# Kernel optimization log

Measured on AMD Instinct MI355X. Metric: run time of the kernel, lower is better.

The kernel has to match this reference:

```python
import jax, jax.numpy as jnp
import numpy as np
import math

V, D, NHEAD, NHID, NLAYERS = 50258, 1024, 8, 2048, 2
NUIDS, B, S, TOPK = 2000, 4, 256, 20


def layer_norm(x, g, b):
    m = x.mean(-1, keepdims=True)
    v = ((x - m) ** 2).mean(-1, keepdims=True)
    return (x - m) / jnp.sqrt(v + 1e-5) * g + b


def mha(x, Wqkv, bqkv, Wo, bo):
    Bx, Sx, Dx = x.shape
    hd = Dx // NHEAD
    qkv = x @ Wqkv.T + bqkv                       # [B,S,3D]
    q, k, v = jnp.split(qkv, 3, axis=-1)
    q = q.reshape(Bx, Sx, NHEAD, hd)
    k = k.reshape(Bx, Sx, NHEAD, hd)
    v = v.reshape(Bx, Sx, NHEAD, hd)
    att = jnp.einsum('bqhd,bkhd->bhqk', q, k) / math.sqrt(hd)
    att = jax.nn.softmax(att, axis=-1)
    o = jnp.einsum('bhqk,bkhd->bqhd', att, v).reshape(Bx, Sx, Dx)
    return o @ Wo.T + bo


def enc_layer(x, Wqkv, bqkv, Wo, bo, W1, b1, W2, b2, g1, be1, g2, be2):
    # torch TransformerEncoderLayer, post-LN, relu, dropout=0 (eval)
    x = layer_norm(x + mha(x, Wqkv, bqkv, Wo, bo), g1, be1)
    ff = jax.nn.relu(x @ W1.T + b1) @ W2.T + b2
    return layer_norm(x + ff, g2, be2)


def setup_inputs() -> dict:
    key = jax.random.key(0)
    ks = jax.random.split(key, 32)
    s = 0.02
    inp = {
        'inputs': jax.random.randint(ks[0], (B, S), 0, V),
        'uids': jnp.arange(NUIDS),
        'noise': jax.random.normal(ks[1], (NUIDS,), dtype=jnp.float32),
        'responses_hidden': jax.random.normal(ks[2], (B, S, D), dtype=jnp.float32),
        'topk': TOPK,
        'emb': jax.random.normal(ks[3], (V, D), dtype=jnp.float32) * s,
        # routing encoder (1 layer)
        'r_Wqkv': jax.random.normal(ks[4], (3 * D, D)) * s,
        'r_bqkv': jnp.zeros((3 * D,)),
        'r_Wo': jax.random.normal(ks[5], (D, D)) * s,
        'r_bo': jnp.zeros((D,)),
        'r_W1': jax.random.normal(ks[6], (NHID, D)) * s,
        'r_b1': jnp.zeros((NHID,)),
        'r_W2': jax.random.normal(ks[7], (D, NHID)) * s,
        'r_b2': jnp.zeros((D,)),
        'r_ln1g': jnp.ones((D,)), 'r_ln1b': jnp.zeros((D,)),
        'r_ln2g': jnp.ones((D,)), 'r_ln2b': jnp.zeros((D,)),
        # main encoder (NLAYERS, stacked)
        'e_Wqkv': jax.random.normal(ks[8], (NLAYERS, 3 * D, D)) * s,
        'e_bqkv': jnp.zeros((NLAYERS, 3 * D)),
        'e_Wo': jax.random.normal(ks[9], (NLAYERS, D, D)) * s,
        'e_bo': jnp.zeros((NLAYERS, D)),
        'e_W1': jax.random.normal(ks[10], (NLAYERS, NHID, D)) * s,
        'e_b1': jnp.zeros((NLAYERS, NHID)),
        'e_W2': jax.random.normal(ks[11], (NLAYERS, D, NHID)) * s,
        'e_b2': jnp.zeros((NLAYERS, D)),
        'e_ln1g': jnp.ones((NLAYERS, D)), 'e_ln1b': jnp.zeros((NLAYERS, D)),
        'e_ln2g': jnp.ones((NLAYERS, D)), 'e_ln2b': jnp.zeros((NLAYERS, D)),
        'dec_W': jax.random.normal(ks[12], (V, D)) * s,
        # 2000 tiny gates fused into one [NUIDS, D] matmul
        'gate_W': jax.random.normal(ks[13], (NUIDS, D)) * s,
        'gate_b': jnp.zeros((NUIDS,)),
    }
    return inp


def reference(inputs, uids, noise, responses_hidden, topk, emb,
              r_Wqkv, r_bqkv, r_Wo, r_bo, r_W1, r_b1, r_W2, r_b2,
              r_ln1g, r_ln1b, r_ln2g, r_ln2b,
              e_Wqkv, e_bqkv, e_Wo, e_bo, e_W1, e_b1, e_W2, e_b2,
              e_ln1g, e_ln1b, e_ln2g, e_ln2b,
              dec_W, gate_W, gate_b):
    # --- routing path ---
    h = emb[inputs]                                            # [B,S,D]
    rc = enc_layer(h, r_Wqkv, r_bqkv, r_Wo, r_bo, r_W1, r_b1,
                   r_W2, r_b2, r_ln1g, r_ln1b, r_ln2g, r_ln2b)
    rc = rc * math.sqrt(D)
    # fused per-UID gates: 2000 Linear(D,1) -> one [B,NUIDS] matmul
    rw = rc[:, -1, :] @ gate_W.T + gate_b                      # [B,NUIDS]
    bw = rw.mean(axis=0)                                       # [NUIDS]
    noisy = noise * jnp.std(bw)
    full = jnp.zeros((NUIDS,), dtype=bw.dtype).at[uids].set(bw + noisy)
    topk_w, topk_uids = jax.lax.top_k(full, topk)
    # --- target loss on joined responses ---
    x = responses_hidden
    for l in range(NLAYERS):
        x = enc_layer(x, e_Wqkv[l], e_bqkv[l], e_Wo[l], e_bo[l],
                      e_W1[l], e_b1[l], e_W2[l], e_b2[l],
                      e_ln1g[l], e_ln1b[l], e_ln2g[l], e_ln2b[l])
    logits = x @ dec_W.T                                       # [B,S,V]
    shift_logits = logits[:, :-1, :].reshape(-1, V)
    shift_labels = inputs[:, 1:].reshape(-1)
    logp = jax.nn.log_softmax(shift_logits, axis=-1)
    loss = -jnp.take_along_axis(logp, shift_labels[:, None], axis=1).mean()
    return loss, topk_w, topk_uids
```

## Files before the change

### kernel.cpp

```cpp
#include <hip/hip_runtime.h>

typedef unsigned short ushort_t;
typedef __bf16 bf16x8_t __attribute__((ext_vector_type(8)));
typedef float f32x4_t __attribute__((ext_vector_type(4)));

#define AS1(p) ((const __attribute__((address_space(1))) void*)(p))
#define AS3(p) ((__attribute__((address_space(3))) void*)(p))
#define DEVINL __device__ __forceinline__

DEVINL ushort_t f2bf(float f) {
    unsigned int u = __builtin_bit_cast(unsigned int, f);
    u += 0x7fffu + ((u >> 16) & 1u);
    return (ushort_t)(u >> 16);
}
DEVINL float bf2f(ushort_t h) {
    unsigned int u = ((unsigned int)h) << 16;
    return __builtin_bit_cast(float, u);
}

DEVINL float warp_sum(float v) {
#pragma unroll
    for (int o = 32; o > 0; o >>= 1) v += __shfl_xor(v, o);
    return v;
}
DEVINL float warp_max(float v) {
#pragma unroll
    for (int o = 32; o > 0; o >>= 1) v = fmaxf(v, __shfl_xor(v, o));
    return v;
}
DEVINL float block_sum(float v, float* sb) {
    v = warp_sum(v);
    int w = threadIdx.x >> 6;
    if ((threadIdx.x & 63) == 0) sb[w] = v;
    __syncthreads();
    v = sb[0] + sb[1] + sb[2] + sb[3];
    __syncthreads();
    return v;
}
DEVINL float block_max(float v, float* sb) {
    v = warp_max(v);
    int w = threadIdx.x >> 6;
    if ((threadIdx.x & 63) == 0) sb[w] = v;
    __syncthreads();
    v = fmaxf(fmaxf(sb[0], sb[1]), fmaxf(sb[2], sb[3]));
    __syncthreads();
    return v;
}

template <int EPI>
__global__ __launch_bounds__(256) void gemm_bt(
    const ushort_t* __restrict__ A, long lda, long sA1, long sA2,
    const ushort_t* __restrict__ B, long ldb, long sB1, long sB2,
    void* __restrict__ Cp, long ldc, long sC1, long sC2,
    const float* __restrict__ bias, int accum, int K, int batch2)
{
    __shared__ __align__(16) __bf16 As[128 * 32];
    __shared__ __align__(16) __bf16 Bs[128 * 32];

    const int tid = threadIdx.x;
    const int lane = tid & 63;
    const int wave = tid >> 6;
    const int wm = wave >> 1, wn = wave & 1;
    const int quad = lane >> 4, l16 = lane & 15;
    const long m0 = (long)blockIdx.y * 128;
    const long n0 = (long)blockIdx.x * 128;
    const int z = blockIdx.z;
    const int z1 = z / batch2, z2 = z % batch2;
    A += (long)z1 * sA1 + (long)z2 * sA2;
    B += (long)z1 * sB1 + (long)z2 * sB2;

    f32x4_t acc[4][4];
#pragma unroll
    for (int i = 0; i < 4; i++)
#pragma unroll
        for (int j = 0; j < 4; j++) {
            f32x4_t zv = {0.f, 0.f, 0.f, 0.f};
            acc[i][j] = zv;
        }

    const int ea = tid * 8;
    const int nkt = K >> 5;
    for (int kt = 0; kt < nkt; ++kt) {
        const int k0 = kt << 5;
#pragma unroll
        for (int inst = 0; inst < 2; ++inst) {
            int e = ea + inst * 2048;
            int row = e >> 5, kk = e & 31;
            __builtin_amdgcn_global_load_lds(AS1(A + (m0 + row) * lda + k0 + kk), AS3(As + e), 16, 0, 0);
            __builtin_amdgcn_global_load_lds(AS1(B + (n0 + row) * ldb + k0 + kk), AS3(Bs + e), 16, 0, 0);
        }
        __syncthreads();
        bf16x8_t af[4], bfr[4];
#pragma unroll
        for (int i = 0; i < 4; i++)
            af[i] = *(const bf16x8_t*)(As + (wm * 64 + i * 16 + l16) * 32 + quad * 8);
#pragma unroll
        for (int j = 0; j < 4; j++)
            bfr[j] = *(const bf16x8_t*)(Bs + (wn * 64 + j * 16 + l16) * 32 + quad * 8);
#pragma unroll
        for (int i = 0; i < 4; i++)
#pragma unroll
            for (int j = 0; j < 4; j++)
                acc[i][j] = __builtin_amdgcn_mfma_f32_16x16x32_bf16(af[i], bfr[j], acc[i][j], 0, 0, 0);
        __syncthreads();
    }

    if constexpr (EPI == 0) {
        float* C = (float*)Cp + (long)z1 * sC1 + (long)z2 * sC2;
#pragma unroll
        for (int i = 0; i < 4; i++)
#pragma unroll
            for (int reg = 0; reg < 4; reg++) {
                long row = m0 + wm * 64 + i * 16 + quad * 4 + reg;
#pragma unroll
                for (int j = 0; j < 4; j++) {
                    long col = n0 + wn * 64 + j * 16 + l16;
                    float v = acc[i][j][reg];
                    if (bias) v += bias[col];
                    long idx = row * ldc + col;
                    if (accum) v += C[idx];
                    C[idx] = v;
                }
            }
    } else {
        ushort_t* C = (ushort_t*)Cp + (long)z1 * sC1 + (long)z2 * sC2;
#pragma unroll
        for (int i = 0; i < 4; i++)
#pragma unroll
            for (int reg = 0; reg < 4; reg++) {
                long row = m0 + wm * 64 + i * 16 + quad * 4 + reg;
#pragma unroll
                for (int j = 0; j < 4; j++) {
                    long col = n0 + wn * 64 + j * 16 + l16;
                    float v = acc[i][j][reg];
                    if (bias) v += bias[col];
                    if constexpr (EPI == 2) v = fmaxf(v, 0.f);
                    C[row * ldc + col] = f2bf(v);
                }
            }
    }
}

__global__ __launch_bounds__(256) void gemm_split(
    const ushort_t* __restrict__ Ah, const ushort_t* __restrict__ Al, long lda,
    const ushort_t* __restrict__ Bh, const ushort_t* __restrict__ Bl, long ldb,
    float* __restrict__ C, long ldc, const float* __restrict__ bias, int K)
{
    __shared__ __align__(16) __bf16 Ahs[4096], Als[4096], Bhs[4096], Bls[4096];
    const int tid = threadIdx.x;
    const int lane = tid & 63;
    const int wave = tid >> 6;
    const int wm = wave >> 1, wn = wave & 1;
    const int quad = lane >> 4, l16 = lane & 15;
    const long m0 = (long)blockIdx.y * 128;
    const long n0 = (long)blockIdx.x * 128;

    f32x4_t acc[4][4];
#pragma unroll
    for (int i = 0; i < 4; i++)
#pragma unroll
        for (int j = 0; j < 4; j++) {
            f32x4_t zv = {0.f, 0.f, 0.f, 0.f};
            acc[i][j] = zv;
        }

    const int ea = tid * 8;
    const int nkt = K >> 5;
    for (int kt = 0; kt < nkt; ++kt) {
        const int k0 = kt << 5;
#pragma unroll
        for (int inst = 0; inst < 2; ++inst) {
            int e = ea + inst * 2048;
            int row = e >> 5, kk = e & 31;
            long ao = (m0 + row) * lda + k0 + kk;
            long bo = (n0 + row) * ldb + k0 + kk;
            __builtin_amdgcn_global_load_lds(AS1(Ah + ao), AS3(Ahs + e), 16, 0, 0);
            __builtin_amdgcn_global_load_lds(AS1(Al + ao), AS3(Als + e), 16, 0, 0);
            __builtin_amdgcn_global_load_lds(AS1(Bh + bo), AS3(Bhs + e), 16, 0, 0);
            __builtin_amdgcn_global_load_lds(AS1(Bl + bo), AS3(Bls + e), 16, 0, 0);
        }
        __syncthreads();
        bf16x8_t ah[4], al[4], bh[4], bl[4];
#pragma unroll
        for (int i = 0; i < 4; i++) {
            int off = (wm * 64 + i * 16 + l16) * 32 + quad * 8;
            ah[i] = *(const bf16x8_t*)(Ahs + off);
            al[i] = *(const bf16x8_t*)(Als + off);
        }
#pragma unroll
        for (int j = 0; j < 4; j++) {
            int off = (wn * 64 + j * 16 + l16) * 32 + quad * 8;
            bh[j] = *(const bf16x8_t*)(Bhs + off);
            bl[j] = *(const bf16x8_t*)(Bls + off);
        }
#pragma unroll
        for (int i = 0; i < 4; i++)
#pragma unroll
            for (int j = 0; j < 4; j++) {
                acc[i][j] = __builtin_amdgcn_mfma_f32_16x16x32_bf16(al[i], bh[j], acc[i][j], 0, 0, 0);
                acc[i][j] = __builtin_amdgcn_mfma_f32_16x16x32_bf16(ah[i], bl[j], acc[i][j], 0, 0, 0);
                acc[i][j] = __builtin_amdgcn_mfma_f32_16x16x32_bf16(ah[i], bh[j], acc[i][j], 0, 0, 0);
            }
        __syncthreads();
    }

#pragma unroll
    for (int i = 0; i < 4; i++)
#pragma unroll
        for (int reg = 0; reg < 4; reg++) {
            long row = m0 + wm * 64 + i * 16 + quad * 4 + reg;
#pragma unroll
            for (int j = 0; j < 4; j++) {
                long col = n0 + wn * 64 + j * 16 + l16;
                C[row * ldc + col] = acc[i][j][reg] + bias[col];
            }
        }
}

__global__ __launch_bounds__(256) void gemm_ce(
    const ushort_t* __restrict__ A, long lda,
    const ushort_t* __restrict__ B, long ldb,
    int K, int n_real, const int* __restrict__ inputs,
    float* __restrict__ part_m, float* __restrict__ part_s,
    float* __restrict__ label_logit)
{
    __shared__ __align__(16) __bf16 As[128 * 32];
    __shared__ __align__(16) __bf16 Bs[128 * 32];

    const int tid = threadIdx.x;
    const int lane = tid & 63;
    const int wave = tid >> 6;
    const int wm = wave >> 1, wn = wave & 1;
    const int quad = lane >> 4, l16 = lane & 15;
    const long m0 = (long)blockIdx.x * 128;
    const long n0 = (long)blockIdx.y * 128;

    f32x4_t acc[4][4];
#pragma unroll
    for (int i = 0; i < 4; i++)
#pragma unroll
        for (int j = 0; j < 4; j++) {
            f32x4_t zv = {0.f, 0.f, 0.f, 0.f};
            acc[i][j] = zv;
        }

    const int ea = tid * 8;
    const int nkt = K >> 5;
    for (int kt = 0; kt < nkt; ++kt) {
        const int k0 = kt << 5;
#pragma unroll
        for (int inst = 0; inst < 2; ++inst) {
            int e = ea + inst * 2048;
            int row = e >> 5, kk = e & 31;
            __builtin_amdgcn_global_load_lds(AS1(A + (m0 + row) * lda + k0 + kk), AS3(As + e), 16, 0, 0);
            __builtin_amdgcn_global_load_lds(AS1(B + (n0 + row) * ldb + k0 + kk), AS3(Bs + e), 16, 0, 0);
        }
        __syncthreads();
        bf16x8_t af[4], bfr[4];
#pragma unroll
        for (int i = 0; i < 4; i++)
            af[i] = *(const bf16x8_t*)(As + (wm * 64 + i * 16 + l16) * 32 + quad * 8);
#pragma unroll
        for (int j = 0; j < 4; j++)
            bfr[j] = *(const bf16x8_t*)(Bs + (wn * 64 + j * 16 + l16) * 32 + quad * 8);
#pragma unroll
        for (int i = 0; i < 4; i++)
#pragma unroll
            for (int j = 0; j < 4; j++)
                acc[i][j] = __builtin_amdgcn_mfma_f32_16x16x32_bf16(af[i], bfr[j], acc[i][j], 0, 0, 0);
        __syncthreads();
    }

#pragma unroll
    for (int i = 0; i < 4; i++) {
#pragma unroll
        for (int reg = 0; reg < 4; reg++) {
            long row = m0 + wm * 64 + i * 16 + quad * 4 + reg;
            int lab = ((row & 255) == 255) ? -1 : inputs[row + 1];
            float mx = -INFINITY;
#pragma unroll
            for (int j = 0; j < 4; j++) {
                long col = n0 + wn * 64 + j * 16 + l16;
                float v = acc[i][j][reg];
                if (col < n_real) mx = fmaxf(mx, v);
            }
#pragma unroll
            for (int o = 8; o > 0; o >>= 1) mx = fmaxf(mx, __shfl_xor(mx, o));
            float sm = 0.f;
#pragma unroll
            for (int j = 0; j < 4; j++) {
                long col = n0 + wn * 64 + j * 16 + l16;
                float v = acc[i][j][reg];
                if (col < n_real) sm += __expf(v - mx);
                if (col == lab) label_logit[row] = v;
            }
#pragma unroll
            for (int o = 8; o > 0; o >>= 1) sm += __shfl_xor(sm, o);
            if (l16 == 0) {
                long pidx = row * 786 + (long)blockIdx.y * 2 + wn;
                part_m[pidx] = mx;
                part_s[pidx] = sm;
            }
        }
    }
}


__global__ __launch_bounds__(256) void k_convert_seg(
    const float* __restrict__ s0, ushort_t* __restrict__ d0, long n0,
    const float* __restrict__ s1, ushort_t* __restrict__ d1, long n1,
    const float* __restrict__ s2, ushort_t* __restrict__ d2, long n2,
    const float* __restrict__ s3, ushort_t* __restrict__ d3, long n3,
    const float* __restrict__ s4, ushort_t* __restrict__ d4, long n4)
{
    long i = ((long)blockIdx.x * 256 + threadIdx.x) * 4;
    const float* src; ushort_t* dst;
    if (i < n0) { src = s0; dst = d0; }
    else if ((i -= n0) < n1) { src = s1; dst = d1; }
    else if ((i -= n1) < n2) { src = s2; dst = d2; }
    else if ((i -= n2) < n3) { src = s3; dst = d3; }
    else if ((i -= n3) < n4) { src = s4; dst = d4; }
    else return;
    float4 v = *(const float4*)(src + i);
    dst[i + 0] = f2bf(v.x); dst[i + 1] = f2bf(v.y);
    dst[i + 2] = f2bf(v.z); dst[i + 3] = f2bf(v.w);
}

__global__ __launch_bounds__(256) void k_convert_pad(const float* __restrict__ src,
                                                     ushort_t* __restrict__ dst,
                                                     long n_src, long n_dst) {
    long i = ((long)blockIdx.x * 256 + threadIdx.x) * 4;
    if (i >= n_dst) return;
    if (i < n_src) {
        float4 v = *(const float4*)(src + i);
        dst[i + 0] = f2bf(v.x); dst[i + 1] = f2bf(v.y);
        dst[i + 2] = f2bf(v.z); dst[i + 3] = f2bf(v.w);
    } else {
        dst[i + 0] = 0; dst[i + 1] = 0; dst[i + 2] = 0; dst[i + 3] = 0;
    }
}

__global__ __launch_bounds__(256) void k_convert2(const float* __restrict__ src,
                                                  ushort_t* __restrict__ hi,
                                                  ushort_t* __restrict__ lo, long n) {
    long i = ((long)blockIdx.x * 256 + threadIdx.x) * 4;
    if (i >= n) return;
    float4 v = *(const float4*)(src + i);
    float vv[4] = {v.x, v.y, v.z, v.w};
#pragma unroll
    for (int j = 0; j < 4; j++) {
        ushort_t h = f2bf(vv[j]);
        hi[i + j] = h;
        lo[i + j] = f2bf(vv[j] - bf2f(h));
    }
}

__global__ __launch_bounds__(256) void k_gather2(const int* __restrict__ inputs,
                                                 const float* __restrict__ emb,
                                                 ushort_t* __restrict__ hi,
                                                 ushort_t* __restrict__ lo,
                                                 float* __restrict__ loss_out) {
    int t = blockIdx.x, tid = threadIdx.x;
    if (t == 0 && tid == 0) loss_out[0] = 0.f;
    long row = inputs[t];
    float4 v = *(const float4*)(emb + row * 1024 + tid * 4);
    long base = (long)t * 1024 + tid * 4;
    float vv[4] = {v.x, v.y, v.z, v.w};
#pragma unroll
    for (int j = 0; j < 4; j++) {
        ushort_t h = f2bf(vv[j]);
        hi[base + j] = h;
        lo[base + j] = f2bf(vv[j] - bf2f(h));
    }
}

__global__ __launch_bounds__(256) void k_rq(
    const int* __restrict__ inputs, const float* __restrict__ emb,
    const float* __restrict__ Wq, const float* __restrict__ bq,
    float* __restrict__ qf)
{
    __shared__ __align__(16) float xs[4096];
    int tid = threadIdx.x;
#pragma unroll
    for (int b2 = 0; b2 < 4; b2++) {
        long tok = inputs[b2 * 256 + 255];
        *(float4*)(xs + b2 * 1024 + tid * 4) = *(const float4*)(emb + tok * 1024 + tid * 4);
    }
    __syncthreads();
    int wave = tid >> 6, lane = tid & 63;
    int d = blockIdx.x * 4 + wave;
    const float4* wr = (const float4*)(Wq + (long)d * 1024) + lane * 4;
    const float4* x0 = (const float4*)xs + lane * 4;
    const float4* x1 = (const float4*)(xs + 1024) + lane * 4;
    const float4* x2 = (const float4*)(xs + 2048) + lane * 4;
    const float4* x3 = (const float4*)(xs + 3072) + lane * 4;
    float a0 = 0, a1 = 0, a2 = 0, a3 = 0;
#pragma unroll
    for (int k = 0; k < 4; k++) {
        float4 w = wr[k];
        float4 v0 = x0[k], v1 = x1[k], v2 = x2[k], v3 = x3[k];
        a0 += w.x * v0.x + w.y * v0.y + w.z * v0.z + w.w * v0.w;
        a1 += w.x * v1.x + w.y * v1.y + w.z * v1.z + w.w * v1.w;
        a2 += w.x * v2.x + w.y * v2.y + w.z * v2.z + w.w * v2.w;
        a3 += w.x * v3.x + w.y * v3.y + w.z * v3.z + w.w * v3.w;
    }
    a0 = warp_sum(a0); a1 = warp_sum(a1); a2 = warp_sum(a2); a3 = warp_sum(a3);
    if (lane < 4) {
        float a = (lane == 0) ? a0 : (lane == 1) ? a1 : (lane == 2) ? a2 : a3;
        qf[lane * 1024 + d] = a + bq[d];
    }
}

__global__ __launch_bounds__(256) void k_rattn(const float* __restrict__ qf,
                                               const float* __restrict__ kv,
                                               float* __restrict__ o_rt) {
    int zz = blockIdx.x, b = zz >> 3, h = zz & 7, tid = threadIdx.x;
    __shared__ __align__(16) float q[128];
    __shared__ float p[256];
    __shared__ float sb[8];
    if (tid < 128) q[tid] = qf[b * 1024 + h * 128 + tid];
    __syncthreads();
    const float4* q4 = (const float4*)q;
    const float4* kr = (const float4*)(kv + ((long)(b * 256 + tid)) * 2048 + h * 128);
    float a = 0.f;
#pragma unroll 8
    for (int k = 0; k < 32; k++) {
        float4 wv = kr[k], xv = q4[k];
        a += wv.x * xv.x + wv.y * xv.y + wv.z * xv.z + wv.w * xv.w;
    }
    a *= 0.08838834764831845f;
    float m = block_max(a, sb);
    float e = __expf(a - m);
    float ssum = block_sum(e, sb);
    p[tid] = e / ssum;
    __syncthreads();
    if (tid < 128) {
        float acc = 0.f;
        const float* vb = kv + (long)b * 256 * 2048 + 1024 + h * 128 + tid;
        for (int s = 0; s < 256; s++) acc += p[s] * vb[(long)s * 2048];
        o_rt[b * 1024 + h * 128 + tid] = acc;
    }
}

__global__ __launch_bounds__(256) void k_rwo(
    const float* __restrict__ o_rt, const int* __restrict__ inputs,
    const float* __restrict__ emb, const float* __restrict__ Wo,
    const float* __restrict__ bo, float* __restrict__ rbuf)
{
    __shared__ __align__(16) float xs[4096];
    int tid = threadIdx.x;
#pragma unroll
    for (int i = 0; i < 16; i++) xs[i * 256 + tid] = o_rt[i * 256 + tid];
    __syncthreads();
    int wave = tid >> 6, lane = tid & 63;
    int d = blockIdx.x * 4 + wave;
    const float4* wr = (const float4*)(Wo + (long)d * 1024) + lane * 4;
    const float4* x0 = (const float4*)xs + lane * 4;
    const float4* x1 = (const float4*)(xs + 1024) + lane * 4;
    const float4* x2 = (const float4*)(xs + 2048) + lane * 4;
    const float4* x3 = (const float4*)(xs + 3072) + lane * 4;
    float a0 = 0, a1 = 0, a2 = 0, a3 = 0;
#pragma unroll
    for (int k = 0; k < 4; k++) {
        float4 w = wr[k];
        float4 v0 = x0[k], v1 = x1[k], v2 = x2[k], v3 = x3[k];
        a0 += w.x * v0.x + w.y * v0.y + w.z * v0.z + w.w * v0.w;
        a1 += w.x * v1.x + w.y * v1.y + w.z * v1.z + w.w * v1.w;
        a2 += w.x * v2.x + w.y * v2.y + w.z * v2.z + w.w * v2.w;
        a3 += w.x * v3.x + w.y * v3.y + w.z * v3.z + w.w * v3.w;
    }
    a0 = warp_sum(a0); a1 = warp_sum(a1); a2 = warp_sum(a2); a3 = warp_sum(a3);
    if (lane < 4) {
        float a = (lane == 0) ? a0 : (lane == 1) ? a1 : (lane == 2) ? a2 : a3;
        long tok = inputs[lane * 256 + 255];
        rbuf[lane * 1024 + d] = emb[tok * 1024 + d] + bo[d] + a;
    }
}

__global__ __launch_bounds__(256) void k_rln(const float* __restrict__ r,
                                             const float* __restrict__ g,
                                             const float* __restrict__ be,
                                             float* __restrict__ outp, float scale) {
    int row = blockIdx.x, tid = threadIdx.x;
    __shared__ float sb[8];
    const float* rr = r + (long)row * 1024;
    float v[4], s = 0.f, sq = 0.f;
#pragma unroll
    for (int i = 0; i < 4; i++) {
        v[i] = rr[i * 256 + tid];
        s += v[i]; sq += v[i] * v[i];
    }
    s = block_sum(s, sb); sq = block_sum(sq, sb + 4);
    float mean = s * (1.f / 1024.f);
    float rstd = rsqrtf(sq * (1.f / 1024.f) - mean * mean + 1e-5f);
#pragma unroll
    for (int i = 0; i < 4; i++) {
        int d = i * 256 + tid;
        outp[(long)row * 1024 + d] = ((v[i] - mean) * rstd * g[d] + be[d]) * scale;
    }
}

__global__ __launch_bounds__(256) void k_rff1(
    const float* __restrict__ x1f, const float* __restrict__ W1,
    const float* __restrict__ b1, float* __restrict__ f1f)
{
    __shared__ __align__(16) float xs[4096];
    int tid = threadIdx.x;
#pragma unroll
    for (int i = 0; i < 16; i++) xs[i * 256 + tid] = x1f[i * 256 + tid];
    __syncthreads();
    int wave = tid >> 6, lane = tid & 63;
    int j = blockIdx.x * 4 + wave;
    const float4* wr = (const float4*)(W1 + (long)j * 1024) + lane * 4;
    const float4* x0 = (const float4*)xs + lane * 4;
    const float4* x1 = (const float4*)(xs + 1024) + lane * 4;
    const float4* x2 = (const float4*)(xs + 2048) + lane * 4;
    const float4* x3 = (const float4*)(xs + 3072) + lane * 4;
    float a0 = 0, a1 = 0, a2 = 0, a3 = 0;
#pragma unroll
    for (int k = 0; k < 4; k++) {
        float4 w = wr[k];
        float4 v0 = x0[k], v1 = x1[k], v2 = x2[k], v3 = x3[k];
        a0 += w.x * v0.x + w.y * v0.y + w.z * v0.z + w.w * v0.w;
        a1 += w.x * v1.x + w.y * v1.y + w.z * v1.z + w.w * v1.w;
        a2 += w.x * v2.x + w.y * v2.y + w.z * v2.z + w.w * v2.w;
        a3 += w.x * v3.x + w.y * v3.y + w.z * v3.z + w.w * v3.w;
    }
    a0 = warp_sum(a0); a1 = warp_sum(a1); a2 = warp_sum(a2); a3 = warp_sum(a3);
    if (lane < 4) {
        float a = (lane == 0) ? a0 : (lane == 1) ? a1 : (lane == 2) ? a2 : a3;
        f1f[lane * 2048 + j] = fmaxf(b1[j] + a, 0.f);
    }
}

__global__ __launch_bounds__(256) void k_rff2(
    const float* __restrict__ f1f, const float* __restrict__ x1f,
    const float* __restrict__ W2, const float* __restrict__ b2,
    float* __restrict__ r2f)
{
    __shared__ __align__(16) float xs[8192];
    int tid = threadIdx.x;
#pragma unroll
    for (int i = 0; i < 32; i++) xs[i * 256 + tid] = f1f[i * 256 + tid];
    __syncthreads();
    int wave = tid >> 6, lane = tid & 63;
    int d = blockIdx.x * 4 + wave;
    const float4* wr = (const float4*)(W2 + (long)d * 2048) + lane * 8;
    const float4* x0 = (const float4*)xs + lane * 8;
    const float4* x1 = (const float4*)(xs + 2048) + lane * 8;
    const float4* x2 = (const float4*)(xs + 4096) + lane * 8;
    const float4* x3 = (const float4*)(xs + 6144) + lane * 8;
    float a0 = 0, a1 = 0, a2 = 0, a3 = 0;
#pragma unroll
    for (int k = 0; k < 8; k++) {
        float4 w = wr[k];
        float4 v0 = x0[k], v1 = x1[k], v2 = x2[k], v3 = x3[k];
        a0 += w.x * v0.x + w.y * v0.y + w.z * v0.z + w.w * v0.w;
        a1 += w.x * v1.x + w.y * v1.y + w.z * v1.z + w.w * v1.w;
        a2 += w.x * v2.x + w.y * v2.y + w.z * v2.z + w.w * v2.w;
        a3 += w.x * v3.x + w.y * v3.y + w.z * v3.z + w.w * v3.w;
    }
    a0 = warp_sum(a0); a1 = warp_sum(a1); a2 = warp_sum(a2); a3 = warp_sum(a3);
    if (lane < 4) {
        float a = (lane == 0) ? a0 : (lane == 1) ? a1 : (lane == 2) ? a2 : a3;
        r2f[lane * 1024 + d] = x1f[lane * 1024 + d] + b2[d] + a;
    }
}

__global__ __launch_bounds__(256) void k_gate(const float* __restrict__ rc,
                                              const float* __restrict__ gw,
                                              const float* __restrict__ gb,
                                              float* __restrict__ bw) {
    __shared__ __align__(16) float xs[4096];
    int tid = threadIdx.x;
#pragma unroll
    for (int i = 0; i < 16; i++) xs[i * 256 + tid] = rc[i * 256 + tid];
    __syncthreads();
    int wave = tid >> 6, lane = tid & 63;
    int u = blockIdx.x * 4 + wave;
    const float4* wr = (const float4*)(gw + (long)u * 1024) + lane * 4;
    const float4* x0 = (const float4*)xs + lane * 4;
    const float4* x1 = (const float4*)(xs + 1024) + lane * 4;
    const float4* x2 = (const float4*)(xs + 2048) + lane * 4;
    const float4* x3 = (const float4*)(xs + 3072) + lane * 4;
    float a0 = 0, a1 = 0, a2 = 0, a3 = 0;
#pragma unroll
    for (int k = 0; k < 4; k++) {
        float4 w = wr[k];
        float4 v0 = x0[k], v1 = x1[k], v2 = x2[k], v3 = x3[k];
        a0 += w.x * v0.x + w.y * v0.y + w.z * v0.z + w.w * v0.w;
        a1 += w.x * v1.x + w.y * v1.y + w.z * v1.z + w.w * v1.w;
        a2 += w.x * v2.x + w.y * v2.y + w.z * v2.z + w.w * v2.w;
        a3 += w.x * v3.x + w.y * v3.y + w.z * v3.z + w.w * v3.w;
    }
    a0 = warp_sum(a0); a1 = warp_sum(a1); a2 = warp_sum(a2); a3 = warp_sum(a3);
    if (lane == 0)
        bw[u] = 0.25f * (a0 + a1 + a2 + a3) + gb[u];
}

__global__ __launch_bounds__(256) void k_topk(const float* __restrict__ bw,
                                              const int* __restrict__ uids,
                                              const float* __restrict__ noise,
                                              float* __restrict__ out) {
    int tid = threadIdx.x;
    __shared__ float full[2000];
    __shared__ float sb[8];
    __shared__ float rv[256];
    __shared__ int ri[256];
    float s = 0.f, sq = 0.f;
    for (int u = tid; u < 2000; u += 256) {
        float v = bw[u];
        s += v; sq += v * v;
    }
    s = block_sum(s, sb); sq = block_sum(sq, sb + 4);
    float mean = s * (1.f / 2000.f);
    float sd = sqrtf(fmaxf(sq * (1.f / 2000.f) - mean * mean, 0.f));
    for (int i = tid; i < 2000; i += 256) full[i] = 0.f;
    __syncthreads();
    for (int i = tid; i < 2000; i += 256) {
        int u = uids[i];
        if (u >= 0 && u < 2000) full[u] = bw[i] + noise[i] * sd;
    }
    __syncthreads();
    for (int it = 0; it < 20; ++it) {
        float bv = -INFINITY;
        int bi = 0x7fffffff;
        for (int i = tid; i < 2000; i += 256) {
            float v = full[i];
            if (v > bv || (v == bv && i < bi)) { bv = v; bi = i; }
        }
        rv[tid] = bv; ri[tid] = bi;
        __syncthreads();
        for (int stride = 128; stride > 0; stride >>= 1) {
            if (tid < stride) {
                float v2 = rv[tid + stride]; int i2 = ri[tid + stride];
                if (v2 > rv[tid] || (v2 == rv[tid] && i2 < ri[tid])) { rv[tid] = v2; ri[tid] = i2; }
            }
            __syncthreads();
        }
        if (tid == 0) {
            out[1 + it] = rv[0];
            out[21 + it] = (float)ri[0];
            full[ri[0]] = -INFINITY;
        }
        __syncthreads();
    }
}

__global__ __launch_bounds__(256) void k_vt(const ushort_t* __restrict__ qkv,
                                            ushort_t* __restrict__ vt) {
    int zz = blockIdx.y, b = zz >> 3, h = zz & 7;
    int s0 = blockIdx.x * 64, tid = threadIdx.x;
    __shared__ ushort_t t[64][130];
#pragma unroll
    for (int r = 0; r < 32; r++) {
        int idx = r * 256 + tid;
        int sl = idx >> 7, d = idx & 127;
        t[sl][d] = qkv[((long)(b * 256 + s0 + sl)) * 3072 + 2048 + h * 128 + d];
    }
    __syncthreads();
#pragma unroll
    for (int r = 0; r < 32; r++) {
        int idx = r * 256 + tid;
        int d = idx >> 6, sl = idx & 63;
        vt[((long)(zz * 128 + d)) * 256 + s0 + sl] = t[sl][d];
    }
}

__global__ void k_softmax(const float* __restrict__ S, ushort_t* __restrict__ P) {
    long row = blockIdx.x;
    int lane = threadIdx.x;
    const float* sr = S + row * 256;
    float v[4];
    float m = -INFINITY;
#pragma unroll
    for (int i = 0; i < 4; i++) {
        v[i] = sr[i * 64 + lane] * 0.08838834764831845f;
        m = fmaxf(m, v[i]);
    }
    m = warp_max(m);
    float s = 0.f;
#pragma unroll
    for (int i = 0; i < 4; i++) { v[i] = __expf(v[i] - m); s += v[i]; }
    s = warp_sum(s);
    float inv = 1.f / s;
#pragma unroll
    for (int i = 0; i < 4; i++) P[row * 256 + i * 64 + lane] = f2bf(v[i] * inv);
}

__global__ __launch_bounds__(256) void k_addln(const float* __restrict__ x,
                                               const float* __restrict__ y,
                                               const float* __restrict__ g,
                                               const float* __restrict__ b,
                                               float* __restrict__ xf,
                                               ushort_t* __restrict__ xb) {
    int row = blockIdx.x, tid = threadIdx.x;
    const float* xr = x + (long)row * 1024;
    const float* yr = y + (long)row * 1024;
    __shared__ float sb[8];
    float r[4], s = 0.f, sq = 0.f;
#pragma unroll
    for (int i = 0; i < 4; i++) {
        int d = i * 256 + tid;
        r[i] = xr[d] + yr[d];
        s += r[i]; sq += r[i] * r[i];
    }
    s = block_sum(s, sb); sq = block_sum(sq, sb + 4);
    float mean = s * (1.f / 1024.f);
    float rstd = rsqrtf(sq * (1.f / 1024.f) - mean * mean + 1e-5f);
#pragma unroll
    for (int i = 0; i < 4; i++) {
        int d = i * 256 + tid;
        float o = (r[i] - mean) * rstd * g[d] + b[d];
        xf[(long)row * 1024 + d] = o;
        xb[(long)row * 1024 + d] = f2bf(o);
    }
}

__global__ __launch_bounds__(256) void k_ce(const float* __restrict__ pm,
                                            const float* __restrict__ ps,
                                            const float* __restrict__ ll,
                                            const int* __restrict__ inputs,
                                            float* __restrict__ out) {
    const int NB = 786;
    long row = blockIdx.x;
    int tid = threadIdx.x;
    __shared__ float sb[8];
    float m = -INFINITY;
    for (int i = tid; i < NB; i += 256) m = fmaxf(m, pm[row * NB + i]);
    m = block_max(m, sb);
    float s = 0.f;
    for (int i = tid; i < NB; i += 256) s += ps[row * NB + i] * __expf(pm[row * NB + i] - m);
    s = block_sum(s, sb);
    if (tid == 0) {
        int lab = ((row & 255) == 255) ? -1 : inputs[row + 1];
        if (lab >= 0) atomicAdd(out, (m + logf(s) - ll[row]) * (1.0f / 1020.0f));
    }
}


extern "C" void kernel_launch(void* const* d_in, const int* in_sizes, int n_in,
                              void* d_out, int out_size, void* d_ws, size_t ws_size,
                              hipStream_t stream) {
    const int* inputs  = (const int*)d_in[0];
    const int* uids    = (const int*)d_in[1];
    const float* noise = (const float*)d_in[2];
    const float* resp  = (const float*)d_in[3];
    const float* emb   = (const float*)d_in[5];
    const float* r_Wqkv = (const float*)d_in[6];
    const float* r_bqkv = (const float*)d_in[7];
    const float* r_Wo = (const float*)d_in[8];
    const float* r_bo = (const float*)d_in[9];
    const float* r_W1 = (const float*)d_in[10];
    const float* r_b1 = (const float*)d_in[11];
    const float* r_W2 = (const float*)d_in[12];
    const float* r_b2 = (const float*)d_in[13];
    const float* r_ln1g = (const float*)d_in[14];
    const float* r_ln1b = (const float*)d_in[15];
    const float* r_ln2g = (const float*)d_in[16];
    const float* r_ln2b = (const float*)d_in[17];
    const float* e_Wqkv = (const float*)d_in[18];
    const float* e_bqkv = (const float*)d_in[19];
    const float* e_Wo = (const float*)d_in[20];
    const float* e_bo = (const float*)d_in[21];
    const float* e_W1 = (const float*)d_in[22];
    const float* e_b1 = (const float*)d_in[23];
    const float* e_W2 = (const float*)d_in[24];
    const float* e_b2 = (const float*)d_in[25];
    const float* e_ln1g = (const float*)d_in[26];
    const float* e_ln1b = (const float*)d_in[27];
    const float* e_ln2g = (const float*)d_in[28];
    const float* e_ln2b = (const float*)d_in[29];
    const float* dec_W = (const float*)d_in[30];
    const float* gate_W = (const float*)d_in[31];
    const float* gate_b = (const float*)d_in[32];
    float* out = (float*)d_out;
    (void)in_sizes; (void)n_in; (void)out_size; (void)ws_size;

    char* wp = (char*)d_ws;
    auto alloc = [&](size_t bytes) {
        char* p = wp;
        wp += (bytes + 255) & ~(size_t)255;
        return p;
    };
    ushort_t* wkv_hi = (ushort_t*)alloc(2097152ull * 2);
    ushort_t* wkv_lo = (ushort_t*)alloc(2097152ull * 2);
    ushort_t* wq_e = (ushort_t*)alloc(6291456ull * 2);
    ushort_t* wo_e = (ushort_t*)alloc(2097152ull * 2);
    ushort_t* w1_e = (ushort_t*)alloc(4194304ull * 2);
    ushort_t* w2_e = (ushort_t*)alloc(4194304ull * 2);
    ushort_t* decb = (ushort_t*)alloc(51511296ull * 2);
    ushort_t* h_hi = (ushort_t*)alloc(1048576ull * 2);
    ushort_t* h_lo = (ushort_t*)alloc(1048576ull * 2);
    float* qf = (float*)alloc(4096ull * 4);
    float* rkv = (float*)alloc(2097152ull * 4);
    float* o_rt = (float*)alloc(4096ull * 4);
    float* rbuf = (float*)alloc(4096ull * 4);
    float* x1f = (float*)alloc(4096ull * 4);
    float* f1f = (float*)alloc(8192ull * 4);
    float* r2f = (float*)alloc(4096ull * 4);
    float* rc = (float*)alloc(4096ull * 4);
    float* bw = (float*)alloc(2000ull * 4);
    ushort_t* xb = (ushort_t*)alloc(1048576ull * 2);
    float* xf = (float*)alloc(1048576ull * 4);
    ushort_t* qkvb = (ushort_t*)alloc(3145728ull * 2);
    ushort_t* vt = (ushort_t*)alloc(1048576ull * 2);
    float* Sb = (float*)alloc(2097152ull * 4);
    ushort_t* Pb = (ushort_t*)alloc(2097152ull * 2);
    ushort_t* ob = (ushort_t*)alloc(1048576ull * 2);
    float* tmpf = (float*)alloc(1048576ull * 4);
    ushort_t* ff1b = (ushort_t*)alloc(2097152ull * 2);
    float* pm = (float*)alloc(1024ull * 786 * 4);
    float* ps = (float*)alloc(1024ull * 786 * 4);
    float* ll = (float*)alloc(1024ull * 4);

    auto gemm = [&](int epi, const ushort_t* A_, long lda_, long sA1_, long sA2_,
                    const ushort_t* B_, long ldb_, long sB1_, long sB2_,
                    void* C_, long ldc_, long sC1_, long sC2_,
                    const float* bias_, int accum_, int M_, int N_, int K_,
                    int batch_, int batch2_) {
        dim3 g((unsigned)(N_ / 128), (unsigned)(M_ / 128), (unsigned)batch_);
        switch (epi) {
        case 0: gemm_bt<0><<<g, 256, 0, stream>>>(A_, lda_, sA1_, sA2_, B_, ldb_, sB1_, sB2_, C_, ldc_, sC1_, sC2_, bias_, accum_, K_, batch2_); break;
        case 1: gemm_bt<1><<<g, 256, 0, stream>>>(A_, lda_, sA1_, sA2_, B_, ldb_, sB1_, sB2_, C_, ldc_, sC1_, sC2_, bias_, accum_, K_, batch2_); break;
        case 2: gemm_bt<2><<<g, 256, 0, stream>>>(A_, lda_, sA1_, sA2_, B_, ldb_, sB1_, sB2_, C_, ldc_, sC1_, sC2_, bias_, accum_, K_, batch2_); break;
        }
    };

    k_convert_seg<<<17408, 256, 0, stream>>>(
        e_Wqkv, wq_e, 6291456L, e_Wo, wo_e, 2097152L, e_W1, w1_e, 4194304L,
        e_W2, w2_e, 4194304L, resp, xb, 1048576L);
    k_convert_pad<<<50304, 256, 0, stream>>>(dec_W, decb, 51464192L, 51511296L);
    k_convert2<<<2048, 256, 0, stream>>>(r_Wqkv + 1048576, wkv_hi, wkv_lo, 2097152L);
    k_gather2<<<1024, 256, 0, stream>>>(inputs, emb, h_hi, h_lo, out);

    k_rq<<<256, 256, 0, stream>>>(inputs, emb, r_Wqkv, r_bqkv, qf);
    {
        dim3 g(16, 8);
        gemm_split<<<g, 256, 0, stream>>>(h_hi, h_lo, 1024, wkv_hi, wkv_lo, 1024,
                                          rkv, 2048, r_bqkv + 1024, 1024);
    }
    k_rattn<<<32, 256, 0, stream>>>(qf, rkv, o_rt);
    k_rwo<<<256, 256, 0, stream>>>(o_rt, inputs, emb, r_Wo, r_bo, rbuf);
    k_rln<<<4, 256, 0, stream>>>(rbuf, r_ln1g, r_ln1b, x1f, 1.0f);
    k_rff1<<<512, 256, 0, stream>>>(x1f, r_W1, r_b1, f1f);
    k_rff2<<<256, 256, 0, stream>>>(f1f, x1f, r_W2, r_b2, r2f);
    k_rln<<<4, 256, 0, stream>>>(r2f, r_ln2g, r_ln2b, rc, 32.0f);
    k_gate<<<500, 256, 0, stream>>>(rc, gate_W, gate_b, bw);
    k_topk<<<1, 256, 0, stream>>>(bw, uids, noise, out);

    for (int l = 0; l < 2; ++l) {
        gemm(1, xb, 1024, 0, 0, wq_e + (size_t)l * 3145728, 1024, 0, 0, qkvb, 3072, 0, 0,
             e_bqkv + l * 3072, 0, 1024, 3072, 1024, 1, 1);
        k_vt<<<dim3(4, 32), 256, 0, stream>>>(qkvb, vt);
        gemm(0, qkvb, 3072, 786432, 128, qkvb + 1024, 3072, 786432, 128, Sb, 256, 524288, 65536,
             nullptr, 0, 256, 256, 128, 32, 8);
        k_softmax<<<8192, 64, 0, stream>>>(Sb, Pb);
        gemm(1, Pb, 256, 524288, 65536, vt, 256, 262144, 32768, ob, 1024, 262144, 128,
             nullptr, 0, 256, 128, 256, 32, 8);
        gemm(0, ob, 1024, 0, 0, wo_e + (size_t)l * 1048576, 1024, 0, 0, tmpf, 1024, 0, 0,
             e_bo + l * 1024, 0, 1024, 1024, 1024, 1, 1);
        k_addln<<<1024, 256, 0, stream>>>((l == 0) ? resp : (const float*)xf, tmpf,
                                          e_ln1g + l * 1024, e_ln1b + l * 1024, xf, xb);
        gemm(2, xb, 1024, 0, 0, w1_e + (size_t)l * 2097152, 1024, 0, 0, ff1b, 2048, 0, 0,
             e_b1 + l * 2048, 0, 1024, 2048, 1024, 1, 1);
        gemm(0, ff1b, 2048, 0, 0, w2_e + (size_t)l * 2097152, 2048, 0, 0, tmpf, 1024, 0, 0,
             e_b2 + l * 1024, 0, 1024, 1024, 2048, 1, 1);
        k_addln<<<1024, 256, 0, stream>>>(xf, tmpf, e_ln2g + l * 1024, e_ln2b + l * 1024, xf, xb);
    }

    {
        dim3 g(8, 393);
        gemm_ce<<<g, 256, 0, stream>>>(xb, 1024, decb, 1024, 1024, 50258, inputs, pm, ps, ll);
    }
    k_ce<<<1024, 256, 0, stream>>>(pm, ps, ll, inputs, out);
}
```

Baseline: 1.272 ms.

## Fuse V-transpose into QKV GEMM, drop CE max pass, merge conversion and LN kernels

```diff
diff --git a/kernel.cpp b/kernel.cpp
--- a/kernel.cpp
+++ b/kernel.cpp
@@ -52,7 +52,8 @@
     const ushort_t* __restrict__ A, long lda, long sA1, long sA2,
     const ushort_t* __restrict__ B, long ldb, long sB1, long sB2,
     void* __restrict__ Cp, long ldc, long sC1, long sC2,
-    const float* __restrict__ bias, int accum, int K, int batch2)
+    const float* __restrict__ bias, int accum, int K, int batch2,
+    ushort_t* __restrict__ vtp)
 {
     __shared__ __align__(16) __bf16 As[128 * 32];
     __shared__ __align__(16) __bf16 Bs[128 * 32];
@@ -120,6 +121,27 @@
                     long idx = row * ldc + col;
                     if (accum) v += C[idx];
                     C[idx] = v;
+                }
+            }
+    } else if constexpr (EPI == 3) {
+        ushort_t* C = (ushort_t*)Cp;
+#pragma unroll
+        for (int i = 0; i < 4; i++)
+#pragma unroll
+            for (int reg = 0; reg < 4; reg++) {
+                long row = m0 + wm * 64 + i * 16 + quad * 4 + reg;
+#pragma unroll
+                for (int j = 0; j < 4; j++) {
+                    long col = n0 + wn * 64 + j * 16 + l16;
+                    float v = acc[i][j][reg];
+                    v += bias[col];
+                    if (col < 2048) {
+                        C[row * ldc + col] = f2bf(v);
+                    } else {
+                        int hc = (int)col - 2048;
+                        long b = row >> 8, s = row & 255;
+                        vtp[(((b * 8) + (hc >> 7)) * 128 + (hc & 127)) * 256 + s] = f2bf(v);
+                    }
                 }
             }
     } else {
@@ -221,11 +243,10 @@
     const ushort_t* __restrict__ A, long lda,
     const ushort_t* __restrict__ B, long ldb,
     int K, int n_real, const int* __restrict__ inputs,
-    float* __restrict__ part_m, float* __restrict__ part_s,
-    float* __restrict__ label_logit)
+    float* __restrict__ part_s, float* __restrict__ label_logit)
 {
-    __shared__ __align__(16) __bf16 As[128 * 32];
-    __shared__ __align__(16) __bf16 Bs[128 * 32];
+    __shared__ __align__(16) __bf16 As[128 * 64];
+    __shared__ __align__(16) __bf16 Bs[128 * 64];
 
     const int tid = threadIdx.x;
     const int lane = tid & 63;
@@ -245,29 +266,32 @@
         }
 
     const int ea = tid * 8;
-    const int nkt = K >> 5;
+    const int nkt = K >> 6;
     for (int kt = 0; kt < nkt; ++kt) {
-        const int k0 = kt << 5;
-#pragma unroll
-        for (int inst = 0; inst < 2; ++inst) {
+        const int k0 = kt << 6;
+#pragma unroll
+        for (int inst = 0; inst < 4; ++inst) {
             int e = ea + inst * 2048;
-            int row = e >> 5, kk = e & 31;
+            int row = e >> 6, kk = e & 63;
             __builtin_amdgcn_global_load_lds(AS1(A + (m0 + row) * lda + k0 + kk), AS3(As + e), 16, 0, 0);
             __builtin_amdgcn_global_load_lds(AS1(B + (n0 + row) * ldb + k0 + kk), AS3(Bs + e), 16, 0, 0);
         }
         __syncthreads();
-        bf16x8_t af[4], bfr[4];
-#pragma unroll
-        for (int i = 0; i < 4; i++)
-            af[i] = *(const bf16x8_t*)(As + (wm * 64 + i * 16 + l16) * 32 + quad * 8);
-#pragma unroll
-        for (int j = 0; j < 4; j++)
-            bfr[j] = *(const bf16x8_t*)(Bs + (wn * 64 + j * 16 + l16) * 32 + quad * 8);
-#pragma unroll
-        for (int i = 0; i < 4; i++)
+#pragma unroll
+        for (int s = 0; s < 2; ++s) {
+            bf16x8_t af[4], bfr[4];
+#pragma unroll
+            for (int i = 0; i < 4; i++)
+                af[i] = *(const bf16x8_t*)(As + (wm * 64 + i * 16 + l16) * 64 + s * 32 + quad * 8);
 #pragma unroll
             for (int j = 0; j < 4; j++)
-                acc[i][j] = __builtin_amdgcn_mfma_f32_16x16x32_bf16(af[i], bfr[j], acc[i][j], 0, 0, 0);
+                bfr[j] = *(const bf16x8_t*)(Bs + (wn * 64 + j * 16 + l16) * 64 + s * 32 + quad * 8);
+#pragma unroll
+            for (int i = 0; i < 4; i++)
+#pragma unroll
+                for (int j = 0; j < 4; j++)
+                    acc[i][j] = __builtin_amdgcn_mfma_f32_16x16x32_bf16(af[i], bfr[j], acc[i][j], 0, 0, 0);
+        }
         __syncthreads();
     }
 
@@ -277,41 +301,30 @@
         for (int reg = 0; reg < 4; reg++) {
             long row = m0 + wm * 64 + i * 16 + quad * 4 + reg;
             int lab = ((row & 255) == 255) ? -1 : inputs[row + 1];
-            float mx = -INFINITY;
+            float sm = 0.f;
 #pragma unroll
             for (int j = 0; j < 4; j++) {
                 long col = n0 + wn * 64 + j * 16 + l16;
                 float v = acc[i][j][reg];
-                if (col < n_real) mx = fmaxf(mx, v);
-            }
-#pragma unroll
-            for (int o = 8; o > 0; o >>= 1) mx = fmaxf(mx, __shfl_xor(mx, o));
-            float sm = 0.f;
-#pragma unroll
-            for (int j = 0; j < 4; j++) {
-                long col = n0 + wn * 64 + j * 16 + l16;
-                float v = acc[i][j][reg];
-                if (col < n_real) sm += __expf(v - mx);
+                if (col < n_real) sm += __expf(v);
                 if (col == lab) label_logit[row] = v;
             }
 #pragma unroll
             for (int o = 8; o > 0; o >>= 1) sm += __shfl_xor(sm, o);
-            if (l16 == 0) {
-                long pidx = row * 786 + (long)blockIdx.y * 2 + wn;
-                part_m[pidx] = mx;
-                part_s[pidx] = sm;
-            }
-        }
-    }
-}
-
-
-__global__ __launch_bounds__(256) void k_convert_seg(
+            if (l16 == 0)
+                part_s[row * 786 + (long)blockIdx.y * 2 + wn] = sm;
+        }
+    }
+}
+
+
+__global__ __launch_bounds__(256) void k_convert_seg6(
     const float* __restrict__ s0, ushort_t* __restrict__ d0, long n0,
     const float* __restrict__ s1, ushort_t* __restrict__ d1, long n1,
     const float* __restrict__ s2, ushort_t* __restrict__ d2, long n2,
     const float* __restrict__ s3, ushort_t* __restrict__ d3, long n3,
-    const float* __restrict__ s4, ushort_t* __restrict__ d4, long n4)
+    const float* __restrict__ s4, ushort_t* __restrict__ d4, long n4,
+    const float* __restrict__ s5, ushort_t* __restrict__ d5, long n5src, long n5dst)
 {
     long i = ((long)blockIdx.x * 256 + threadIdx.x) * 4;
     const float* src; ushort_t* dst;
@@ -320,24 +333,14 @@
     else if ((i -= n1) < n2) { src = s2; dst = d2; }
     else if ((i -= n2) < n3) { src = s3; dst = d3; }
     else if ((i -= n3) < n4) { src = s4; dst = d4; }
+    else if ((i -= n4) < n5dst) {
+        if (i < n5src) { src = s5; dst = d5; }
+        else { d5[i] = 0; d5[i + 1] = 0; d5[i + 2] = 0; d5[i + 3] = 0; return; }
+    }
     else return;
     float4 v = *(const float4*)(src + i);
     dst[i + 0] = f2bf(v.x); dst[i + 1] = f2bf(v.y);
     dst[i + 2] = f2bf(v.z); dst[i + 3] = f2bf(v.w);
-}
-
-__global__ __launch_bounds__(256) void k_convert_pad(const float* __restrict__ src,
-                                                     ushort_t* __restrict__ dst,
-                                                     long n_src, long n_dst) {
-    long i = ((long)blockIdx.x * 256 + threadIdx.x) * 4;
-    if (i >= n_dst) return;
-    if (i < n_src) {
-        float4 v = *(const float4*)(src + i);
-        dst[i + 0] = f2bf(v.x); dst[i + 1] = f2bf(v.y);
-        dst[i + 2] = f2bf(v.z); dst[i + 3] = f2bf(v.w);
-    } else {
-        dst[i + 0] = 0; dst[i + 1] = 0; dst[i + 2] = 0; dst[i + 3] = 0;
-    }
 }
 
 __global__ __launch_bounds__(256) void k_convert2(const float* __restrict__ src,
@@ -477,38 +480,45 @@
     }
 }
 
-__global__ __launch_bounds__(256) void k_rln(const float* __restrict__ r,
-                                             const float* __restrict__ g,
-                                             const float* __restrict__ be,
-                                             float* __restrict__ outp, float scale) {
-    int row = blockIdx.x, tid = threadIdx.x;
-    __shared__ float sb[8];
-    const float* rr = r + (long)row * 1024;
-    float v[4], s = 0.f, sq = 0.f;
-#pragma unroll
-    for (int i = 0; i < 4; i++) {
-        v[i] = rr[i * 256 + tid];
-        s += v[i]; sq += v[i] * v[i];
-    }
-    s = block_sum(s, sb); sq = block_sum(sq, sb + 4);
-    float mean = s * (1.f / 1024.f);
-    float rstd = rsqrtf(sq * (1.f / 1024.f) - mean * mean + 1e-5f);
-#pragma unroll
-    for (int i = 0; i < 4; i++) {
-        int d = i * 256 + tid;
-        outp[(long)row * 1024 + d] = ((v[i] - mean) * rstd * g[d] + be[d]) * scale;
-    }
+DEVINL void ln4_inplace(float* xs, const float* __restrict__ g,
+                        const float* __restrict__ be, float scale, float* sb) {
+    int tid = threadIdx.x;
+    float ls[4] = {0, 0, 0, 0}, lq[4] = {0, 0, 0, 0};
+#pragma unroll
+    for (int i = 0; i < 16; i++) {
+        float v = xs[i * 256 + tid];
+        int r = i >> 2;
+        ls[r] += v; lq[r] += v * v;
+    }
+    float mean[4], rstd[4];
+#pragma unroll
+    for (int r = 0; r < 4; r++) {
+        float S = block_sum(ls[r], sb);
+        float Q = block_sum(lq[r], sb + 4);
+        mean[r] = S * (1.f / 1024.f);
+        rstd[r] = rsqrtf(Q * (1.f / 1024.f) - mean[r] * mean[r] + 1e-5f);
+    }
+#pragma unroll
+    for (int i = 0; i < 16; i++) {
+        int r = i >> 2, d = (i & 3) * 256 + tid;
+        float v = xs[i * 256 + tid];
+        xs[i * 256 + tid] = ((v - mean[r]) * rstd[r] * g[d] + be[d]) * scale;
+    }
+    __syncthreads();
 }
 
 __global__ __launch_bounds__(256) void k_rff1(
-    const float* __restrict__ x1f, const float* __restrict__ W1,
+    const float* __restrict__ rbuf, const float* __restrict__ g1,
+    const float* __restrict__ be1, const float* __restrict__ W1,
     const float* __restrict__ b1, float* __restrict__ f1f)
 {
     __shared__ __align__(16) float xs[4096];
+    __shared__ float sb[8];
     int tid = threadIdx.x;
 #pragma unroll
-    for (int i = 0; i < 16; i++) xs[i * 256 + tid] = x1f[i * 256 + tid];
-    __syncthreads();
+    for (int i = 0; i < 16; i++) xs[i * 256 + tid] = rbuf[i * 256 + tid];
+    __syncthreads();
+    ln4_inplace(xs, g1, be1, 1.0f, sb);
     int wave = tid >> 6, lane = tid & 63;
     int j = blockIdx.x * 4 + wave;
     const float4* wr = (const float4*)(W1 + (long)j * 1024) + lane * 4;
@@ -534,15 +544,21 @@
 }
 
 __global__ __launch_bounds__(256) void k_rff2(
-    const float* __restrict__ f1f, const float* __restrict__ x1f,
+    const float* __restrict__ f1f, const float* __restrict__ rbuf,
+    const float* __restrict__ g1, const float* __restrict__ be1,
     const float* __restrict__ W2, const float* __restrict__ b2,
     float* __restrict__ r2f)
 {
     __shared__ __align__(16) float xs[8192];
+    __shared__ __align__(16) float x1s[4096];
+    __shared__ float sb[8];
     int tid = threadIdx.x;
 #pragma unroll
     for (int i = 0; i < 32; i++) xs[i * 256 + tid] = f1f[i * 256 + tid];
-    __syncthreads();
+#pragma unroll
+    for (int i = 0; i < 16; i++) x1s[i * 256 + tid] = rbuf[i * 256 + tid];
+    __syncthreads();
+    ln4_inplace(x1s, g1, be1, 1.0f, sb);
     int wave = tid >> 6, lane = tid & 63;
     int d = blockIdx.x * 4 + wave;
     const float4* wr = (const float4*)(W2 + (long)d * 2048) + lane * 8;
@@ -563,19 +579,23 @@
     a0 = warp_sum(a0); a1 = warp_sum(a1); a2 = warp_sum(a2); a3 = warp_sum(a3);
     if (lane < 4) {
         float a = (lane == 0) ? a0 : (lane == 1) ? a1 : (lane == 2) ? a2 : a3;
-        r2f[lane * 1024 + d] = x1f[lane * 1024 + d] + b2[d] + a;
-    }
-}
-
-__global__ __launch_bounds__(256) void k_gate(const float* __restrict__ rc,
+        r2f[lane * 1024 + d] = x1s[lane * 1024 + d] + b2[d] + a;
+    }
+}
+
+__global__ __launch_bounds__(256) void k_gate(const float* __restrict__ r2f,
+                                              const float* __restrict__ g2,
+                                              const float* __restrict__ be2,
                                               const float* __restrict__ gw,
                                               const float* __restrict__ gb,
                                               float* __restrict__ bw) {
     __shared__ __align__(16) float xs[4096];
+    __shared__ float sb[8];
     int tid = threadIdx.x;
 #pragma unroll
-    for (int i = 0; i < 16; i++) xs[i * 256 + tid] = rc[i * 256 + tid];
-    __syncthreads();
+    for (int i = 0; i < 16; i++) xs[i * 256 + tid] = r2f[i * 256 + tid];
+    __syncthreads();
+    ln4_inplace(xs, g2, be2, 32.0f, sb);
     int wave = tid >> 6, lane = tid & 63;
     int u = blockIdx.x * 4 + wave;
     const float4* wr = (const float4*)(gw + (long)u * 1024) + lane * 4;
@@ -647,26 +667,6 @@
     }
 }
 
-__global__ __launch_bounds__(256) void k_vt(const ushort_t* __restrict__ qkv,
-                                            ushort_t* __restrict__ vt) {
-    int zz = blockIdx.y, b = zz >> 3, h = zz & 7;
-    int s0 = blockIdx.x * 64, tid = threadIdx.x;
-    __shared__ ushort_t t[64][130];
-#pragma unroll
-    for (int r = 0; r < 32; r++) {
-        int idx = r * 256 + tid;
-        int sl = idx >> 7, d = idx & 127;
-        t[sl][d] = qkv[((long)(b * 256 + s0 + sl)) * 3072 + 2048 + h * 128 + d];
-    }
-    __syncthreads();
-#pragma unroll
-    for (int r = 0; r < 32; r++) {
-        int idx = r * 256 + tid;
-        int d = idx >> 6, sl = idx & 63;
-        vt[((long)(zz * 128 + d)) * 256 + s0 + sl] = t[sl][d];
-    }
-}
-
 __global__ void k_softmax(const float* __restrict__ S, ushort_t* __restrict__ P) {
     long row = blockIdx.x;
     int lane = threadIdx.x;
@@ -717,8 +717,7 @@
     }
 }
 
-__global__ __launch_bounds__(256) void k_ce(const float* __restrict__ pm,
-                                            const float* __restrict__ ps,
+__global__ __launch_bounds__(256) void k_ce(const float* __restrict__ ps,
                                             const float* __restrict__ ll,
                                             const int* __restrict__ inputs,
                                             float* __restrict__ out) {
@@ -726,15 +725,12 @@
     long row = blockIdx.x;
     int tid = threadIdx.x;
     __shared__ float sb[8];
-    float m = -INFINITY;
-    for (int i = tid; i < NB; i += 256) m = fmaxf(m, pm[row * NB + i]);
-    m = block_max(m, sb);
     float s = 0.f;
-    for (int i = tid; i < NB; i += 256) s += ps[row * NB + i] * __expf(pm[row * NB + i] - m);
+    for (int i = tid; i < NB; i += 256) s += ps[row * NB + i];
     s = block_sum(s, sb);
     if (tid == 0) {
         int lab = ((row & 255) == 255) ? -1 : inputs[row + 1];
-        if (lab >= 0) atomicAdd(out, (m + logf(s) - ll[row]) * (1.0f / 1020.0f));
+        if (lab >= 0) atomicAdd(out, (logf(s) - ll[row]) * (1.0f / 1020.0f));
     }
 }
 
@@ -796,10 +792,8 @@
     float* rkv = (float*)alloc(2097152ull * 4);
     float* o_rt = (float*)alloc(4096ull * 4);
     float* rbuf = (float*)alloc(4096ull * 4);
-    float* x1f = (float*)alloc(4096ull * 4);
     float* f1f = (float*)alloc(8192ull * 4);
     float* r2f = (float*)alloc(4096ull * 4);
-    float* rc = (float*)alloc(4096ull * 4);
     float* bw = (float*)alloc(2000ull * 4);
     ushort_t* xb = (ushort_t*)alloc(1048576ull * 2);
     float* xf = (float*)alloc(1048576ull * 4);
@@ -810,7 +804,6 @@
     ushort_t* ob = (ushort_t*)alloc(1048576ull * 2);
     float* tmpf = (float*)alloc(1048576ull * 4);
     ushort_t* ff1b = (ushort_t*)alloc(2097152ull * 2);
-    float* pm = (float*)alloc(1024ull * 786 * 4);
     float* ps = (float*)alloc(1024ull * 786 * 4);
     float* ll = (float*)alloc(1024ull * 4);
 
@@ -818,19 +811,20 @@
                     const ushort_t* B_, long ldb_, long sB1_, long sB2_,
                     void* C_, long ldc_, long sC1_, long sC2_,
                     const float* bias_, int accum_, int M_, int N_, int K_,
-                    int batch_, int batch2_) {
+                    int batch_, int batch2_, ushort_t* vtp_) {
         dim3 g((unsigned)(N_ / 128), (unsigned)(M_ / 128), (unsigned)batch_);
         switch (epi) {
-        case 0: gemm_bt<0><<<g, 256, 0, stream>>>(A_, lda_, sA1_, sA2_, B_, ldb_, sB1_, sB2_, C_, ldc_, sC1_, sC2_, bias_, accum_, K_, batch2_); break;
-        case 1: gemm_bt<1><<<g, 256, 0, stream>>>(A_, lda_, sA1_, sA2_, B_, ldb_, sB1_, sB2_, C_, ldc_, sC1_, sC2_, bias_, accum_, K_, batch2_); break;
-        case 2: gemm_bt<2><<<g, 256, 0, stream>>>(A_, lda_, sA1_, sA2_, B_, ldb_, sB1_, sB2_, C_, ldc_, sC1_, sC2_, bias_, accum_, K_, batch2_); break;
+        case 0: gemm_bt<0><<<g, 256, 0, stream>>>(A_, lda_, sA1_, sA2_, B_, ldb_, sB1_, sB2_, C_, ldc_, sC1_, sC2_, bias_, accum_, K_, batch2_, vtp_); break;
+        case 1: gemm_bt<1><<<g, 256, 0, stream>>>(A_, lda_, sA1_, sA2_, B_, ldb_, sB1_, sB2_, C_, ldc_, sC1_, sC2_, bias_, accum_, K_, batch2_, vtp_); break;
+        case 2: gemm_bt<2><<<g, 256, 0, stream>>>(A_, lda_, sA1_, sA2_, B_, ldb_, sB1_, sB2_, C_, ldc_, sC1_, sC2_, bias_, accum_, K_, batch2_, vtp_); break;
+        case 3: gemm_bt<3><<<g, 256, 0, stream>>>(A_, lda_, sA1_, sA2_, B_, ldb_, sB1_, sB2_, C_, ldc_, sC1_, sC2_, bias_, accum_, K_, batch2_, vtp_); break;
         }
     };
 
-    k_convert_seg<<<17408, 256, 0, stream>>>(
+    k_convert_seg6<<<67712, 256, 0, stream>>>(
         e_Wqkv, wq_e, 6291456L, e_Wo, wo_e, 2097152L, e_W1, w1_e, 4194304L,
-        e_W2, w2_e, 4194304L, resp, xb, 1048576L);
-    k_convert_pad<<<50304, 256, 0, stream>>>(dec_W, decb, 51464192L, 51511296L);
+        e_W2, w2_e, 4194304L, resp, xb, 1048576L,
+        dec_W, decb, 51464192L, 51511296L);
     k_convert2<<<2048, 256, 0, stream>>>(r_Wqkv + 1048576, wkv_hi, wkv_lo, 2097152L);
     k_gather2<<<1024, 256, 0, stream>>>(inputs, emb, h_hi, h_lo, out);
 
@@ -842,36 +836,33 @@
     }
     k_rattn<<<32, 256, 0, stream>>>(qf, rkv, o_rt);
     k_rwo<<<256, 256, 0, stream>>>(o_rt, inputs, emb, r_Wo, r_bo, rbuf);
-    k_rln<<<4, 256, 0, stream>>>(rbuf, r_ln1g, r_ln1b, x1f, 1.0f);
-    k_rff1<<<512, 256, 0, stream>>>(x1f, r_W1, r_b1, f1f);
-    k_rff2<<<256, 256, 0, stream>>>(f1f, x1f, r_W2, r_b2, r2f);
-    k_rln<<<4, 256, 0, stream>>>(r2f, r_ln2g, r_ln2b, rc, 32.0f);
-    k_gate<<<500, 256, 0, stream>>>(rc, gate_W, gate_b, bw);
+    k_rff1<<<512, 256, 0, stream>>>(rbuf, r_ln1g, r_ln1b, r_W1, r_b1, f1f);
+    k_rff2<<<256, 256, 0, stream>>>(f1f, rbuf, r_ln1g, r_ln1b, r_W2, r_b2, r2f);
+    k_gate<<<500, 256, 0, stream>>>(r2f, r_ln2g, r_ln2b, gate_W, gate_b, bw);
     k_topk<<<1, 256, 0, stream>>>(bw, uids, noise, out);
 
     for (int l = 0; l < 2; ++l) {
-        gemm(1, xb, 1024, 0, 0, wq_e + (size_t)l * 3145728, 1024, 0, 0, qkvb, 3072, 0, 0,
-             e_bqkv + l * 3072, 0, 1024, 3072, 1024, 1, 1);
-        k_vt<<<dim3(4, 32), 256, 0, stream>>>(qkvb, vt);
+        gemm(3, xb, 1024, 0, 0, wq_e + (size_t)l * 3145728, 1024, 0, 0, qkvb, 3072, 0, 0,
+             e_bqkv + l * 3072, 0, 1024, 3072, 1024, 1, 1, vt);
         gemm(0, qkvb, 3072, 786432, 128, qkvb + 1024, 3072, 786432, 128, Sb, 256, 524288, 65536,
-             nullptr, 0, 256, 256, 128, 32, 8);
+             nullptr, 0, 256, 256, 128, 32, 8, nullptr);
         k_softmax<<<8192, 64, 0, stream>>>(Sb, Pb);
         gemm(1, Pb, 256, 524288, 65536, vt, 256, 262144, 32768, ob, 1024, 262144, 128,
-             nullptr, 0, 256, 128, 256, 32, 8);
+             nullptr, 0, 256, 128, 256, 32, 8, nullptr);
         gemm(0, ob, 1024, 0, 0, wo_e + (size_t)l * 1048576, 1024, 0, 0, tmpf, 1024, 0, 0,
-             e_bo + l * 1024, 0, 1024, 1024, 1024, 1, 1);
+             e_bo + l * 1024, 0, 1024, 1024, 1024, 1, 1, nullptr);
         k_addln<<<1024, 256, 0, stream>>>((l == 0) ? resp : (const float*)xf, tmpf,
                                           e_ln1g + l * 1024, e_ln1b + l * 1024, xf, xb);
         gemm(2, xb, 1024, 0, 0, w1_e + (size_t)l * 2097152, 1024, 0, 0, ff1b, 2048, 0, 0,
-             e_b1 + l * 2048, 0, 1024, 2048, 1024, 1, 1);
+             e_b1 + l * 2048, 0, 1024, 2048, 1024, 1, 1, nullptr);
         gemm(0, ff1b, 2048, 0, 0, w2_e + (size_t)l * 2097152, 2048, 0, 0, tmpf, 1024, 0, 0,
-             e_b2 + l * 1024, 0, 1024, 1024, 2048, 1, 1);
+             e_b2 + l * 1024, 0, 1024, 1024, 2048, 1, 1, nullptr);
         k_addln<<<1024, 256, 0, stream>>>(xf, tmpf, e_ln2g + l * 1024, e_ln2b + l * 1024, xf, xb);
     }
 
     {
         dim3 g(8, 393);
-        gemm_ce<<<g, 256, 0, stream>>>(xb, 1024, decb, 1024, 1024, 50258, inputs, pm, ps, ll);
-    }
-    k_ce<<<1024, 256, 0, stream>>>(pm, ps, ll, inputs, out);
-}
+        gemm_ce<<<g, 256, 0, stream>>>(xb, 1024, decb, 1024, 1024, 50258, inputs, ps, ll);
+    }
+    k_ce<<<1024, 256, 0, stream>>>(ps, ll, inputs, out);
+}
```

Result: no change. 1.273 ms (+0.1%).
